# Kernel optimization log

Measured on AMD Instinct MI355X. Metric: run time of the kernel, lower is better.

The kernel has to match this reference:

```python
import jax, jax.numpy as jnp
import numpy as np
from jax import lax

SD = 16  # sample_duration
POOL_KS = (SD, SD * 3 // 4, SD // 2, SD // 4)  # (16, 12, 8, 4)


def conv3d_same(x, w, b):
    # x: [B,C,T,H,W], w: [O,I,3,3,3]
    y = lax.conv_general_dilated(
        x, w, window_strides=(1, 1, 1), padding=[(1, 1), (1, 1), (1, 1)],
        dimension_numbers=("NCDHW", "OIDHW", "NCDHW"))
    return y + b[None, :, None, None, None]


def maxpool_t(x, k):
    # MaxPool3d((k,1,1), stride=1): max over sliding temporal window
    return lax.reduce_window(x, -jnp.inf, lax.max,
                             (1, 1, k, 1, 1), (1, 1, 1, 1, 1), "VALID")


def head1x1(x, w, b):
    # 1x1x1 Conv3d as einsum; x: [B,C,T,H,W], w: [O,C]
    return jnp.einsum("bcthw,oc->bothw", x, w) + b[None, :, None, None, None]


def cls_prob(score):
    # _RPN.reshape(x,2) -> softmax(dim=1) -> reshape back to [B,30,T,H,W]
    B, C, T, H, W = score.shape
    s2 = score.reshape(B, 2, (C * T) // 2, H, W)
    p = jax.nn.softmax(s2, axis=1)
    return p.reshape(B, C, T, H, W)


def setup_inputs() -> dict:
    key = jax.random.key(0)
    ks = jax.random.split(key, 12)
    din, B, H, W = 512, 2, 28, 28
    s = 0.05
    return {
        "base_feat": jax.random.normal(ks[0], (B, din, SD, H, W), jnp.float32),
        "im_info": jnp.ones((B, 3), jnp.float32) * 448.0,
        "gt_boxes": jax.random.uniform(ks[1], (B, 20, 5), jnp.float32),
        "gt_rois": jax.random.uniform(ks[2], (B, 20, SD, 5), jnp.float32),
        "W_conv": jax.random.normal(ks[3], (din, din, 3, 3, 3), jnp.float32) * 0.01,
        "b_conv": jnp.zeros((din,), jnp.float32),
        "W_cls": jax.random.normal(ks[4], (30, din), jnp.float32) * s,
        "b_cls": jnp.zeros((30,), jnp.float32),
        "W_bbox": jax.random.normal(ks[5], (960, din), jnp.float32) * s,
        "b_bbox": jnp.zeros((960,), jnp.float32),
        "W_bbox_34": jax.random.normal(ks[6], (720, din), jnp.float32) * s,
        "b_bbox_34": jnp.zeros((720,), jnp.float32),
        "W_bbox_2": jax.random.normal(ks[7], (480, din), jnp.float32) * s,
        "b_bbox_2": jnp.zeros((480,), jnp.float32),
        "W_bbox_4": jax.random.normal(ks[8], (240, din), jnp.float32) * s,
        "b_bbox_4": jnp.zeros((240,), jnp.float32),
    }


def reference(base_feat, im_info, gt_boxes, gt_rois,
              W_conv, b_conv, W_cls, b_cls,
              W_bbox, b_bbox, W_bbox_34, b_bbox_34,
              W_bbox_2, b_bbox_2, W_bbox_4, b_bbox_4):
    # RPN conv + relu
    x = jax.nn.relu(conv3d_same(base_feat, W_conv, b_conv))
    # four temporal max-pool branches (T' = 1, 5, 9, 13)
    pools = [maxpool_t(x, k) for k in POOL_KS]
    # NOTE: original code applies the SAME RPN_cls_score conv to all branches
    probs = tuple(cls_prob(head1x1(p, W_cls, b_cls)) for p in pools)
    bbox_ws = [(W_bbox, b_bbox), (W_bbox_34, b_bbox_34),
               (W_bbox_2, b_bbox_2), (W_bbox_4, b_bbox_4)]
    bboxes = tuple(head1x1(p, w, b) for p, (w, b) in zip(pools, bbox_ws))
    return probs + bboxes
```

## Files before the change

### kernel.cpp

```cpp
#include <hip/hip_runtime.h>

typedef unsigned short u16;
typedef unsigned int   u32;
typedef __bf16  bf16x8 __attribute__((ext_vector_type(8)));
typedef float   f32x4  __attribute__((ext_vector_type(4)));

__device__ __forceinline__ float bf2f(u16 u) {
    u32 v = ((u32)u) << 16;
    return __builtin_bit_cast(float, v);
}
__device__ __forceinline__ u16 f2bf(float f) {
    u32 u = __builtin_bit_cast(u32, f);
    return (u16)((u + 0x7FFFu + ((u >> 16) & 1u)) >> 16);
}
__device__ __forceinline__ float ldf(const void* p, long i, int f32) {
    return f32 ? ((const float*)p)[i] : bf2f(((const u16*)p)[i]);
}
__device__ __forceinline__ int is_f32(const u32* im) {
    return im[0] == 0x43E00000u;
}
__device__ __forceinline__ void gl2lds16(const u16* g, u16* l) {
    __builtin_amdgcn_global_load_lds(
        (const __attribute__((address_space(1))) void*)g,
        (__attribute__((address_space(3))) void*)l, 16, 0, 0);
}

__global__ void pad_zero_fill(const void* __restrict__ src, u16* __restrict__ xpad,
                              const u32* __restrict__ im)
{
    __shared__ u16 lds[56 * 40];
    if (blockIdx.x >= 7168) {
        int i = (blockIdx.x - 7168) * 256 + threadIdx.x;
        if (i < 230400) {
            int c8 = i & 63; int pos = i >> 6;
            int p = pos % 900; pos /= 900;
            int t = (pos & 1) * 17; int b = pos >> 1;
            long o = (((long)(b * 18 + t) * 900) + p) * 512 + c8 * 8;
            *(uint4*)&xpad[o] = uint4{0u, 0u, 0u, 0u};
            return;
        }
        i -= 230400;
        if (i < 122880) {
            int c8 = i & 63; int pos = i >> 6;
            int w = pos % 30; pos /= 30;
            int h = (pos & 1) * 29; pos >>= 1;
            int t = pos % 16 + 1; int b = pos / 16;
            long o = ((((long)(b * 18 + t) * 30 + h) * 30) + w) * 512 + c8 * 8;
            *(uint4*)&xpad[o] = uint4{0u, 0u, 0u, 0u};
            return;
        }
        i -= 122880;
        if (i < 114688) {
            int c8 = i & 63; int pos = i >> 6;
            int w = (pos & 1) * 29; pos >>= 1;
            int h = pos % 28 + 1; pos /= 28;
            int t = pos % 16 + 1; int b = pos / 16;
            long o = ((((long)(b * 18 + t) * 30 + h) * 30) + w) * 512 + c8 * 8;
            *(uint4*)&xpad[o] = uint4{0u, 0u, 0u, 0u};
        }
        return;
    }
    const int f32 = is_f32(im);
    int blk = blockIdx.x;
    const int h2  = blk % 14;  blk /= 14;
    const int c32 = blk & 15;  blk >>= 4;
    const int t   = blk & 15;
    const int b   = blk >> 4;
    const int tid = threadIdx.x;
    const long sbase = ((long)(b * 512 + c32 * 32) * 16 + t) * 784 + h2 * 56;
    #pragma unroll
    for (int it = tid; it < 1792; it += 256) {
        const int c = it / 56, p = it - c * 56;
        float v = f32 ? ((const float*)src)[sbase + (long)c * 12544 + p]
                      : bf2f(((const u16*)src)[sbase + (long)c * 12544 + p]);
        lds[p * 40 + c] = f2bf(v);
    }
    __syncthreads();
    if (tid < 224) {
        const int p = tid >> 2, g = tid & 3;
        const int h = h2 * 2 + p / 28, w = p % 28;
        const long o = (((long)(b * 18 + t + 1) * 30 + h + 1) * 30 + (w + 1)) * 512
                       + c32 * 32 + g * 8;
        *(uint4*)&xpad[o] = *(const uint4*)&lds[p * 40 + g * 8];
    }
}

__global__ void wt_cvt_all(const void* __restrict__ wconv, u16* __restrict__ wt,
                           const void* s0, const void* s1, const void* s2,
                           const void* s3, const void* s4,
                           const void* b0, const void* b1, const void* b2,
                           const void* b3, const void* b4, const void* b5,
                           u16* __restrict__ whd, float* __restrict__ bfs,
                           const u32* __restrict__ im)
{
    const int f32 = is_f32(im);
    __shared__ u16 lds[256 * 28];
    const int tid = threadIdx.x;
    if (blockIdx.x < 1024) {
        const int pair_base = blockIdx.x * 256;
        const long s0l = (long)pair_base * 27;
        for (int it = tid; it < 256 * 27; it += 256) {
            const int p = it / 27, o = it - p * 27;
            float v = f32 ? ((const float*)wconv)[s0l + it]
                          : bf2f(((const u16*)wconv)[s0l + it]);
            lds[p * 28 + o] = f2bf(v);
        }
        __syncthreads();
        #pragma unroll
        for (int off = 0; off < 27; ++off)
            wt[(long)off * 262144 + pair_base + tid] = lds[tid * 28 + off];
        return;
    }
    int i = (blockIdx.x - 1024) * 256 + tid;
    if (i < 1244160) {
        const void* s; long j;
        if      (i < 15360)   { s = s0; j = i; }
        else if (i < 506880)  { s = s1; j = i - 15360; }
        else if (i < 875520)  { s = s2; j = i - 506880; }
        else if (i < 1121280) { s = s3; j = i - 875520; }
        else                  { s = s4; j = i - 1121280; }
        whd[i] = f2bf(ldf(s, j, f32));
        return;
    }
    i -= 1244160;
    if (i >= 2942) return;
    float v;
    if      (i < 512)  v = ldf(b0, i, f32);
    else if (i < 542)  v = ldf(b1, i - 512, f32);
    else if (i < 1502) v = ldf(b2, i - 542, f32);
    else if (i < 2222) v = ldf(b3, i - 1502, f32);
    else if (i < 2702) v = ldf(b4, i - 2222, f32);
    else               v = ldf(b5, i - 2702, f32);
    bfs[i] = v;
}

__global__ __launch_bounds__(512, 2) void conv_gemm256(
    const u16* __restrict__ xpad, const u16* __restrict__ wt,
    const float* __restrict__ bfs, u16* __restrict__ y)
{
    __shared__ u16 smem[61440];
    const int tid = threadIdx.x;

    const int bx  = blockIdx.x;
    const int L   = (bx & 7) * 28 + (bx >> 3);
    const int m_base = (L & 1) * 256;
    const int n_base = (L >> 1) * 224;

    const int rq8 = tid >> 3;
    const int sw  = (((tid & 7) ^ (rq8 & 7))) * 8;
    const u16* pa = wt + (long)(m_base + rq8) * 512 + sw;

    long sbj[4];
    #pragma unroll
    for (int j = 0; j < 4; ++j) {
        int n = n_base + j * 56 + rq8;
        if (n > 25087) n = 25087;
        int b = n / 12544, r = n % 12544;
        int t = r / 784,   q = r % 784;
        int h = q / 28,    w = q % 28;
        const int sa = ((b * 18 + t) * 30 + h) * 30 + w;
        sbj[j] = (long)sa * 512 + sw;
    }
    const bool stgB = (tid < 448);

    const int lane = tid & 63, wid = tid >> 6;
    const int l16 = lane & 15, quad = lane >> 4;
    const int wm = wid >> 1;
    const int wn = wid & 1;
    const int x7 = l16 & 7;
    const int o0 = (quad ^ x7) * 8;
    const int o1 = ((4 + quad) ^ x7) * 8;
    int rowA[4], rowB[7];
    #pragma unroll
    for (int mi = 0; mi < 4; ++mi) rowA[mi] = (wm * 64 + mi * 16 + l16) * 64;
    #pragma unroll
    for (int ni = 0; ni < 7; ++ni) rowB[ni] = 16384 + (wn * 112 + ni * 16 + l16) * 64;

    f32x4 acc[4][7] = {};

    {
        u16* dst = smem;
        #pragma unroll
        for (int j = 0; j < 4; ++j)
            gl2lds16(pa + (long)j * 32768, dst + j * 4096 + tid * 8);
        if (stgB) {
            #pragma unroll
            for (int j = 0; j < 4; ++j)
                gl2lds16(xpad + sbj[j], dst + 16384 + j * 3584 + tid * 8);
        }
    }

    for (int kt = 0; kt < 216; ++kt) {
        asm volatile("s_waitcnt vmcnt(0)" ::: "memory");
        asm volatile("s_barrier" ::: "memory");
        const u16* buf = smem + (kt & 1) * 30720;

        bf16x8 af[4], bfr[7];
        #pragma unroll
        for (int mi = 0; mi < 4; ++mi)
            af[mi] = *(const bf16x8*)&buf[rowA[mi] + o0];
        #pragma unroll
        for (int ni = 0; ni < 7; ++ni)
            bfr[ni] = *(const bf16x8*)&buf[rowB[ni] + o0];

        if (kt < 215) {
            const int kts = kt + 1;
            const int tap = kts >> 3, kc = kts & 7;
            const int kd = tap / 9, r9 = tap - kd * 9;
            const int kh = r9 / 3,  kw = r9 - kh * 3;
            const long aoff = (long)tap * 262144 + kc * 64;
            const long boff = (long)(kd * 900 + kh * 30 + kw) * 512 + kc * 64;
            u16* dst = smem + (kts & 1) * 30720;
            #pragma unroll
            for (int j = 0; j < 4; ++j)
                gl2lds16(pa + aoff + (long)j * 32768, dst + j * 4096 + tid * 8);
            if (stgB) {
                #pragma unroll
                for (int j = 0; j < 4; ++j)
                    gl2lds16(xpad + sbj[j] + boff, dst + 16384 + j * 3584 + tid * 8);
            }
        }

        __builtin_amdgcn_s_setprio(1);
        #pragma unroll
        for (int mi = 0; mi < 4; ++mi)
            #pragma unroll
            for (int ni = 0; ni < 7; ++ni)
                acc[mi][ni] = __builtin_amdgcn_mfma_f32_16x16x32_bf16(
                    af[mi], bfr[ni], acc[mi][ni], 0, 0, 0);
        __builtin_amdgcn_s_setprio(0);

        bf16x8 ag[4], bgr[7];
        #pragma unroll
        for (int mi = 0; mi < 4; ++mi)
            ag[mi] = *(const bf16x8*)&buf[rowA[mi] + o1];
        #pragma unroll
        for (int ni = 0; ni < 7; ++ni)
            bgr[ni] = *(const bf16x8*)&buf[rowB[ni] + o1];

        __builtin_amdgcn_s_setprio(1);
        #pragma unroll
        for (int mi = 0; mi < 4; ++mi)
            #pragma unroll
            for (int ni = 0; ni < 7; ++ni)
                acc[mi][ni] = __builtin_amdgcn_mfma_f32_16x16x32_bf16(
                    ag[mi], bgr[ni], acc[mi][ni], 0, 0, 0);
        __builtin_amdgcn_s_setprio(0);
    }

    #pragma unroll
    for (int mi = 0; mi < 4; ++mi) {
        const int mrow = m_base + wm * 64 + mi * 16 + quad * 4;
        float bias[4];
        #pragma unroll
        for (int r = 0; r < 4; ++r) bias[r] = bfs[mrow + r];
        #pragma unroll
        for (int ni = 0; ni < 7; ++ni) {
            const int ng = n_base + wn * 112 + ni * 16 + l16;
            f32x4 a = acc[mi][ni];
            u16 o0v = f2bf(fmaxf(a[0] + bias[0], 0.f));
            u16 o1v = f2bf(fmaxf(a[1] + bias[1], 0.f));
            u16 o2v = f2bf(fmaxf(a[2] + bias[2], 0.f));
            u16 o3v = f2bf(fmaxf(a[3] + bias[3], 0.f));
            uint2 pv;
            pv.x = (u32)o0v | ((u32)o1v << 16);
            pv.y = (u32)o2v | ((u32)o3v << 16);
            *(uint2*)&y[(long)ng * 512 + mrow] = pv;
        }
    }
}

__device__ __forceinline__ uint2 max4(uint2 A, uint2 Bv)
{
    const u16* a = (const u16*)&A;
    const u16* b = (const u16*)&Bv;
    uint2 R;
    u16* r = (u16*)&R;
    #pragma unroll
    for (int i = 0; i < 4; ++i) r[i] = (bf2f(a[i]) >= bf2f(b[i])) ? a[i] : b[i];
    return R;
}

__global__ void pool_all(const u16* __restrict__ y, u16* __restrict__ p4,
                         u16* __restrict__ p8, u16* __restrict__ p12,
                         u16* __restrict__ p16)
{
    int g = blockIdx.x * 256 + threadIdx.x;
    if (g >= 200704) return;
    const int c4 = g & 127;
    int pos = g >> 7;
    const int hw = pos % 784; const int b = pos / 784;
    const u16* src = y + ((long)(b * 16) * 784 + hw) * 512 + c4 * 4;
    uint2 v[16];
    #pragma unroll
    for (int t = 0; t < 16; ++t)
        v[t] = *(const uint2*)(src + (long)t * 401408);
    uint2 pr[15];
    #pragma unroll
    for (int t = 0; t < 15; ++t) pr[t] = max4(v[t], v[t + 1]);
    uint2 qd[13];
    #pragma unroll
    for (int t = 0; t < 13; ++t) qd[t] = max4(pr[t], pr[t + 2]);
    uint2 e8[9];
    #pragma unroll
    for (int t = 0; t < 9; ++t) e8[t] = max4(qd[t], qd[t + 4]);
    uint2 e12[5];
    #pragma unroll
    for (int t = 0; t < 5; ++t) e12[t] = max4(e8[t], qd[t + 8]);
    uint2 e16 = max4(e8[0], e8[8]);

    const long col = (long)hw * 512 + c4 * 4;
    #pragma unroll
    for (int t = 0; t < 13; ++t)
        *(uint2*)&p4[((long)(b * 13 + t) * 784) * 512 + col] = qd[t];
    #pragma unroll
    for (int t = 0; t < 9; ++t)
        *(uint2*)&p8[((long)(b * 9 + t) * 784) * 512 + col] = e8[t];
    #pragma unroll
    for (int t = 0; t < 5; ++t)
        *(uint2*)&p12[((long)(b * 5 + t) * 784) * 512 + col] = e12[t];
    *(uint2*)&p16[((long)b * 784) * 512 + col] = e16;
}

__global__ __launch_bounds__(256, 2) void heads_gemm(
    const u16* __restrict__ p16, const u16* __restrict__ p12,
    const u16* __restrict__ p8,  const u16* __restrict__ p4,
    const u16* __restrict__ wcls, const u16* __restrict__ wb1,
    const u16* __restrict__ wb34, const u16* __restrict__ wb2,
    const u16* __restrict__ wb4,  const float* __restrict__ bfs,
    void* __restrict__ outv, const u32* __restrict__ im)
{
    const int f32 = is_f32(im);
    int bid = blockIdx.x;
    const u16* pool; const u16* wbp; int Ti, CH, nt, mt; long boff, coff, ooff;
    if (bid < 104)      {             nt = bid % 13;  mt = bid / 13;  pool = p16; wbp = wb1;  Ti = 1;  CH = 960; boff = 542;  coff = 0;      ooff = 1317120; }
    else if (bid < 476) { bid -= 104; nt = bid % 62;  mt = bid / 62;  pool = p12; wbp = wb34; Ti = 5;  CH = 720; boff = 1502; coff = 47040;  ooff = 2822400; }
    else if (bid < 920) { bid -= 476; nt = bid % 111; mt = bid / 111; pool = p8;  wbp = wb2;  Ti = 9;  CH = 480; boff = 2222; coff = 282240; ooff = 8467200; }
    else                { bid -= 920; nt = bid % 160; mt = bid / 160; pool = p4;  wbp = wb4;  Ti = 13; CH = 240; boff = 2702; coff = 705600; ooff = 15240960; }
    const int M = 30 + CH;
    const int THW = Ti * 784;
    const int N = 2 * THW;
    const int n_base = nt * 128;
    const int m_base = mt * 128;

    __shared__ u16 lds[24576];
    const int tid = threadIdx.x;
    const int lane = tid & 63;
    const int wid  = tid >> 6;
    const int quad = lane >> 4;
    const int l16  = lane & 15;
    const int wm = (wid & 1) * 64;
    const int wn = (wid >> 1) * 64;

    const int srow = tid >> 2;
    const int kk   = (((tid & 3) ^ ((tid >> 3) & 3))) * 8;

    const u16* arow[2]; const u16* brow[2];
    #pragma unroll
    for (int i = 0; i < 2; ++i) {
        int m = m_base + i * 64 + srow; if (m > M - 1) m = M - 1;
        arow[i] = ((m < 30) ? (wcls + m * 512) : (wbp + (m - 30) * 512)) + kk;
        int n = n_base + i * 64 + srow; if (n > N - 1) n = N - 1;
        brow[i] = pool + (long)n * 512 + kk;
    }

    const int co = (quad ^ ((l16 >> 1) & 3)) * 8;
    int rowA[4], rowB[4];
    #pragma unroll
    for (int i = 0; i < 4; ++i) {
        rowA[i] = (wm + i * 16 + l16) * 32 + co;
        rowB[i] = 4096 + (wn + i * 16 + l16) * 32 + co;
    }

    #pragma unroll
    for (int i = 0; i < 2; ++i)
        gl2lds16(arow[i], &lds[i * 2048 + tid * 8]);
    #pragma unroll
    for (int i = 0; i < 2; ++i)
        gl2lds16(brow[i], &lds[4096 + i * 2048 + tid * 8]);
    #pragma unroll
    for (int i = 0; i < 2; ++i)
        gl2lds16(arow[i] + 32, &lds[8192 + i * 2048 + tid * 8]);
    #pragma unroll
    for (int i = 0; i < 2; ++i)
        gl2lds16(brow[i] + 32, &lds[8192 + 4096 + i * 2048 + tid * 8]);

    f32x4 acc[4][4] = {};
    int cb = 0;
    for (int kc = 0; kc < 15; ++kc) {
        asm volatile("s_waitcnt vmcnt(4)" ::: "memory");
        asm volatile("s_barrier" ::: "memory");
        const u16* buf = lds + cb * 8192;
        bf16x8 af[4], bfr[4];
        #pragma unroll
        for (int mi = 0; mi < 4; ++mi)
            af[mi]  = *(const bf16x8*)&buf[rowA[mi]];
        #pragma unroll
        for (int ni = 0; ni < 4; ++ni)
            bfr[ni] = *(const bf16x8*)&buf[rowB[ni]];
        if (kc < 14) {
            const int kcol = (kc + 2) * 32;
            int nb = cb + 2; if (nb >= 3) nb -= 3;
            u16* dst = lds + nb * 8192 + tid * 8;
            #pragma unroll
            for (int i = 0; i < 2; ++i)
                gl2lds16(arow[i] + kcol, dst + i * 2048);
            #pragma unroll
            for (int i = 0; i < 2; ++i)
                gl2lds16(brow[i] + kcol, dst + 4096 + i * 2048);
        }
        __builtin_amdgcn_s_setprio(1);
        #pragma unroll
        for (int mi = 0; mi < 4; ++mi)
            #pragma unroll
            for (int ni = 0; ni < 4; ++ni)
                acc[mi][ni] = __builtin_amdgcn_mfma_f32_16x16x32_bf16(
                    af[mi], bfr[ni], acc[mi][ni], 0, 0, 0);
        __builtin_amdgcn_s_setprio(0);
        cb = (cb + 1 == 3) ? 0 : cb + 1;
    }
    {
        asm volatile("s_waitcnt vmcnt(0)" ::: "memory");
        asm volatile("s_barrier" ::: "memory");
        const u16* buf = lds + cb * 8192;
        bf16x8 af[4], bfr[4];
        #pragma unroll
        for (int mi = 0; mi < 4; ++mi)
            af[mi]  = *(const bf16x8*)&buf[rowA[mi]];
        #pragma unroll
        for (int ni = 0; ni < 4; ++ni)
            bfr[ni] = *(const bf16x8*)&buf[rowB[ni]];
        #pragma unroll
        for (int mi = 0; mi < 4; ++mi)
            #pragma unroll
            for (int ni = 0; ni < 4; ++ni)
                acc[mi][ni] = __builtin_amdgcn_mfma_f32_16x16x32_bf16(
                    af[mi], bfr[ni], acc[mi][ni], 0, 0, 0);
    }

    __syncthreads();
    float* smf = (float*)lds;
    const float* bcls = bfs + 512;
    const float* bb   = bfs + boff;
    #pragma unroll
    for (int mi = 0; mi < 4; ++mi) {
        const int mrow = m_base + wm + mi * 16 + quad * 4;
        #pragma unroll
        for (int ni = 0; ni < 4; ++ni) {
            const int ng = n_base + wn + ni * 16 + l16;
            if (ng >= N) continue;
            const int b  = ng / THW;
            const int rr = ng % THW;
            f32x4 a = acc[mi][ni];
            #pragma unroll
            for (int r = 0; r < 4; ++r) {
                const int m = mrow + r;
                if (m >= M) break;
                if (m < 30) {
                    smf[m * 128 + (wn + ni * 16 + l16)] = a[r] + bcls[m];
                } else {
                    const float v = a[r] + bb[m - 30];
                    const long oi = ooff + ((long)(b * CH + (m - 30))) * THW + rr;
                    if (f32) ((float*)outv)[oi] = v;
                    else     ((u16*)outv)[oi]   = f2bf(v);
                }
            }
        }
    }
    __syncthreads();
    if (m_base == 0) {
        for (int p = tid; p < 1920; p += 256) {
            const int j = p >> 7, col = p & 127;
            const int ng = n_base + col;
            if (ng >= N) continue;
            const float s0 = smf[j * 128 + col];
            const float s1 = smf[(j + 15) * 128 + col];
            const float mx = fmaxf(s0, s1);
            const float e0 = __expf(s0 - mx), e1 = __expf(s1 - mx);
            const float inv = 1.0f / (e0 + e1);
            const int b = ng / THW, rr = ng % THW;
            const long i0 = coff + ((long)(b * 30 + j)) * THW + rr;
            const long i1 = coff + ((long)(b * 30 + j + 15)) * THW + rr;
            if (f32) {
                ((float*)outv)[i0] = e0 * inv;
                ((float*)outv)[i1] = e1 * inv;
            } else {
                ((u16*)outv)[i0] = f2bf(e0 * inv);
                ((u16*)outv)[i1] = f2bf(e1 * inv);
            }
        }
    }
}

extern "C" void kernel_launch(void* const* d_in, const int* in_sizes, int n_in,
                              void* d_out, int out_size, void* d_ws, size_t ws_size,
                              hipStream_t stream)
{
    const void* base_feat = d_in[0];
    const u32*  im_info   = (const u32*)d_in[1];
    const void* W_conv    = d_in[4];
    const void* b_conv    = d_in[5];
    const void* W_cls     = d_in[6];
    const void* b_cls     = d_in[7];
    const void* W_bbox    = d_in[8];
    const void* b_bbox    = d_in[9];
    const void* W_bbox34  = d_in[10];
    const void* b_bbox34  = d_in[11];
    const void* W_bbox2   = d_in[12];
    const void* b_bbox2   = d_in[13];
    const void* W_bbox4   = d_in[14];
    const void* b_bbox4   = d_in[15];

    char* ws = (char*)d_ws;
    u16*   xpad = (u16*)  (ws + 0);
    u16*   wt   = (u16*)  (ws + 33177600);
    u16*   y    = (u16*)  (ws + 47333376);
    u16*   p4   = (u16*)  (ws + 73023488);
    u16*   p8   = (u16*)  (ws + 93896704);
    u16*   p12  = (u16*)  (ws + 108347392);
    u16*   p16  = (u16*)  (ws + 116375552);
    u16*   whd  = (u16*)  (ws + 123249728);
    float* bfs  = (float*)(ws + 125738048);

    u16* w_cls_b  = whd;
    u16* w_b1_b   = whd + 15360;
    u16* w_b34_b  = whd + 506880;
    u16* w_b2_b   = whd + 875520;
    u16* w_b4_b   = whd + 1121280;

    pad_zero_fill<<<8996, 256, 0, stream>>>(base_feat, xpad, im_info);
    wt_cvt_all<<<5897, 256, 0, stream>>>(W_conv, wt,
                                         W_cls, W_bbox, W_bbox34, W_bbox2, W_bbox4,
                                         b_conv, b_cls, b_bbox, b_bbox34, b_bbox2,
                                         b_bbox4, whd, bfs, im_info);

    conv_gemm256<<<224, 512, 0, stream>>>(xpad, wt, bfs, y);

    pool_all<<<784, 256, 0, stream>>>(y, p4, p8, p12, p16);

    heads_gemm<<<1400, 256, 0, stream>>>(p16, p12, p8, p4,
                                         w_cls_b, w_b1_b, w_b34_b, w_b2_b, w_b4_b,
                                         bfs, d_out, im_info);
}
```

Measured before the change: 541.9 us.

## Merge prep kernels and enlarge heads GEMM M-tile to 256

Merges the input padding/zero-fill kernel and the weight conversion kernel into a single launch, removing one kernel launch and its tail. The heads GEMM now uses 256x128 tiles instead of 128x128, so each wave computes 128x64 with 8x4 MFMA accumulators. This roughly halves the number of blocks and cuts re-reads of the pooled activations, at the cost of more registers and LDS (72KB). It also wastes more compute on padded M rows for the small-channel branches.

```diff
diff --git a/kernel.cpp b/kernel.cpp
--- a/kernel.cpp
+++ b/kernel.cpp
@@ -25,12 +25,44 @@
         (__attribute__((address_space(3))) void*)l, 16, 0, 0);
 }
 
-__global__ void pad_zero_fill(const void* __restrict__ src, u16* __restrict__ xpad,
-                              const u32* __restrict__ im)
+__global__ void prep_all(const void* __restrict__ src, u16* __restrict__ xpad,
+                         const void* __restrict__ wconv, u16* __restrict__ wt,
+                         const void* s0, const void* s1, const void* s2,
+                         const void* s3, const void* s4,
+                         const void* b0, const void* b1, const void* b2,
+                         const void* b3, const void* b4, const void* b5,
+                         u16* __restrict__ whd, float* __restrict__ bfs,
+                         const u32* __restrict__ im)
 {
-    __shared__ u16 lds[56 * 40];
-    if (blockIdx.x >= 7168) {
-        int i = (blockIdx.x - 7168) * 256 + threadIdx.x;
+    __shared__ u16 lds[7168];
+    const int tid = threadIdx.x;
+    if (blockIdx.x < 7168) {
+        const int f32 = is_f32(im);
+        int blk = blockIdx.x;
+        const int h2  = blk % 14;  blk /= 14;
+        const int c32 = blk & 15;  blk >>= 4;
+        const int t   = blk & 15;
+        const int b   = blk >> 4;
+        const long sbase = ((long)(b * 512 + c32 * 32) * 16 + t) * 784 + h2 * 56;
+        #pragma unroll
+        for (int it = tid; it < 1792; it += 256) {
+            const int c = it / 56, p = it - c * 56;
+            float v = f32 ? ((const float*)src)[sbase + (long)c * 12544 + p]
+                          : bf2f(((const u16*)src)[sbase + (long)c * 12544 + p]);
+            lds[p * 40 + c] = f2bf(v);
+        }
+        __syncthreads();
+        if (tid < 224) {
+            const int p = tid >> 2, g = tid & 3;
+            const int h = h2 * 2 + p / 28, w = p % 28;
+            const long o = (((long)(b * 18 + t + 1) * 30 + h + 1) * 30 + (w + 1)) * 512
+                           + c32 * 32 + g * 8;
+            *(uint4*)&xpad[o] = *(const uint4*)&lds[p * 40 + g * 8];
+        }
+        return;
+    }
+    if (blockIdx.x < 8996) {
+        int i = (blockIdx.x - 7168) * 256 + tid;
         if (i < 230400) {
             int c8 = i & 63; int pos = i >> 6;
             int p = pos % 900; pos /= 900;
@@ -61,43 +93,8 @@
         return;
     }
     const int f32 = is_f32(im);
-    int blk = blockIdx.x;
-    const int h2  = blk % 14;  blk /= 14;
-    const int c32 = blk & 15;  blk >>= 4;
-    const int t   = blk & 15;
-    const int b   = blk >> 4;
-    const int tid = threadIdx.x;
-    const long sbase = ((long)(b * 512 + c32 * 32) * 16 + t) * 784 + h2 * 56;
-    #pragma unroll
-    for (int it = tid; it < 1792; it += 256) {
-        const int c = it / 56, p = it - c * 56;
-        float v = f32 ? ((const float*)src)[sbase + (long)c * 12544 + p]
-                      : bf2f(((const u16*)src)[sbase + (long)c * 12544 + p]);
-        lds[p * 40 + c] = f2bf(v);
-    }
-    __syncthreads();
-    if (tid < 224) {
-        const int p = tid >> 2, g = tid & 3;
-        const int h = h2 * 2 + p / 28, w = p % 28;
-        const long o = (((long)(b * 18 + t + 1) * 30 + h + 1) * 30 + (w + 1)) * 512
-                       + c32 * 32 + g * 8;
-        *(uint4*)&xpad[o] = *(const uint4*)&lds[p * 40 + g * 8];
-    }
-}
-
-__global__ void wt_cvt_all(const void* __restrict__ wconv, u16* __restrict__ wt,
-                           const void* s0, const void* s1, const void* s2,
-                           const void* s3, const void* s4,
-                           const void* b0, const void* b1, const void* b2,
-                           const void* b3, const void* b4, const void* b5,
-                           u16* __restrict__ whd, float* __restrict__ bfs,
-                           const u32* __restrict__ im)
-{
-    const int f32 = is_f32(im);
-    __shared__ u16 lds[256 * 28];
-    const int tid = threadIdx.x;
-    if (blockIdx.x < 1024) {
-        const int pair_base = blockIdx.x * 256;
+    if (blockIdx.x < 10020) {
+        const int pair_base = (blockIdx.x - 8996) * 256;
         const long s0l = (long)pair_base * 27;
         for (int it = tid; it < 256 * 27; it += 256) {
             const int p = it / 27, o = it - p * 27;
@@ -111,7 +108,7 @@
             wt[(long)off * 262144 + pair_base + tid] = lds[tid * 28 + off];
         return;
     }
-    int i = (blockIdx.x - 1024) * 256 + tid;
+    int i = (blockIdx.x - 10020) * 256 + tid;
     if (i < 1244160) {
         const void* s; long j;
         if      (i < 15360)   { s = s0; j = i; }
@@ -333,67 +330,69 @@
     const int f32 = is_f32(im);
     int bid = blockIdx.x;
     const u16* pool; const u16* wbp; int Ti, CH, nt, mt; long boff, coff, ooff;
-    if (bid < 104)      {             nt = bid % 13;  mt = bid / 13;  pool = p16; wbp = wb1;  Ti = 1;  CH = 960; boff = 542;  coff = 0;      ooff = 1317120; }
-    else if (bid < 476) { bid -= 104; nt = bid % 62;  mt = bid / 62;  pool = p12; wbp = wb34; Ti = 5;  CH = 720; boff = 1502; coff = 47040;  ooff = 2822400; }
-    else if (bid < 920) { bid -= 476; nt = bid % 111; mt = bid / 111; pool = p8;  wbp = wb2;  Ti = 9;  CH = 480; boff = 2222; coff = 282240; ooff = 8467200; }
-    else                { bid -= 920; nt = bid % 160; mt = bid / 160; pool = p4;  wbp = wb4;  Ti = 13; CH = 240; boff = 2702; coff = 705600; ooff = 15240960; }
+    if (bid < 52)       {             nt = bid % 13;  mt = bid / 13;  pool = p16; wbp = wb1;  Ti = 1;  CH = 960; boff = 542;  coff = 0;      ooff = 1317120; }
+    else if (bid < 238) { bid -= 52;  nt = bid % 62;  mt = bid / 62;  pool = p12; wbp = wb34; Ti = 5;  CH = 720; boff = 1502; coff = 47040;  ooff = 2822400; }
+    else if (bid < 460) { bid -= 238; nt = bid % 111; mt = bid / 111; pool = p8;  wbp = wb2;  Ti = 9;  CH = 480; boff = 2222; coff = 282240; ooff = 8467200; }
+    else                { bid -= 460; nt = bid % 160; mt = bid / 160; pool = p4;  wbp = wb4;  Ti = 13; CH = 240; boff = 2702; coff = 705600; ooff = 15240960; }
     const int M = 30 + CH;
     const int THW = Ti * 784;
     const int N = 2 * THW;
     const int n_base = nt * 128;
-    const int m_base = mt * 128;
-
-    __shared__ u16 lds[24576];
+    const int m_base = mt * 256;
+
+    __shared__ u16 lds[36864];
     const int tid = threadIdx.x;
     const int lane = tid & 63;
     const int wid  = tid >> 6;
     const int quad = lane >> 4;
     const int l16  = lane & 15;
-    const int wm = (wid & 1) * 64;
-    const int wn = (wid >> 1) * 64;
+    const int wm = wid & 1;
+    const int wn = wid >> 1;
 
     const int srow = tid >> 2;
     const int kk   = (((tid & 3) ^ ((tid >> 3) & 3))) * 8;
 
-    const u16* arow[2]; const u16* brow[2];
-    #pragma unroll
-    for (int i = 0; i < 2; ++i) {
+    const u16* arow[4]; const u16* brow[2];
+    #pragma unroll
+    for (int i = 0; i < 4; ++i) {
         int m = m_base + i * 64 + srow; if (m > M - 1) m = M - 1;
         arow[i] = ((m < 30) ? (wcls + m * 512) : (wbp + (m - 30) * 512)) + kk;
+    }
+    #pragma unroll
+    for (int i = 0; i < 2; ++i) {
         int n = n_base + i * 64 + srow; if (n > N - 1) n = N - 1;
         brow[i] = pool + (long)n * 512 + kk;
     }
 
     const int co = (quad ^ ((l16 >> 1) & 3)) * 8;
-    int rowA[4], rowB[4];
-    #pragma unroll
-    for (int i = 0; i < 4; ++i) {
-        rowA[i] = (wm + i * 16 + l16) * 32 + co;
-        rowB[i] = 4096 + (wn + i * 16 + l16) * 32 + co;
-    }
-
-    #pragma unroll
-    for (int i = 0; i < 2; ++i)
-        gl2lds16(arow[i], &lds[i * 2048 + tid * 8]);
-    #pragma unroll
-    for (int i = 0; i < 2; ++i)
-        gl2lds16(brow[i], &lds[4096 + i * 2048 + tid * 8]);
-    #pragma unroll
-    for (int i = 0; i < 2; ++i)
-        gl2lds16(arow[i] + 32, &lds[8192 + i * 2048 + tid * 8]);
-    #pragma unroll
-    for (int i = 0; i < 2; ++i)
-        gl2lds16(brow[i] + 32, &lds[8192 + 4096 + i * 2048 + tid * 8]);
-
-    f32x4 acc[4][4] = {};
+    int rowA[8], rowB[4];
+    #pragma unroll
+    for (int i = 0; i < 8; ++i)
+        rowA[i] = (wm * 128 + i * 16 + l16) * 32 + co;
+    #pragma unroll
+    for (int i = 0; i < 4; ++i)
+        rowB[i] = 8192 + (wn * 64 + i * 16 + l16) * 32 + co;
+
+    #pragma unroll
+    for (int s = 0; s < 2; ++s) {
+        u16* dst = lds + s * 12288 + tid * 8;
+        #pragma unroll
+        for (int i = 0; i < 4; ++i)
+            gl2lds16(arow[i] + s * 32, dst + i * 2048);
+        #pragma unroll
+        for (int i = 0; i < 2; ++i)
+            gl2lds16(brow[i] + s * 32, dst + 8192 + i * 2048);
+    }
+
+    f32x4 acc[8][4] = {};
     int cb = 0;
     for (int kc = 0; kc < 15; ++kc) {
-        asm volatile("s_waitcnt vmcnt(4)" ::: "memory");
+        asm volatile("s_waitcnt vmcnt(6)" ::: "memory");
         asm volatile("s_barrier" ::: "memory");
-        const u16* buf = lds + cb * 8192;
-        bf16x8 af[4], bfr[4];
-        #pragma unroll
-        for (int mi = 0; mi < 4; ++mi)
+        const u16* buf = lds + cb * 12288;
+        bf16x8 af[8], bfr[4];
+        #pragma unroll
+        for (int mi = 0; mi < 8; ++mi)
             af[mi]  = *(const bf16x8*)&buf[rowA[mi]];
         #pragma unroll
         for (int ni = 0; ni < 4; ++ni)
@@ -401,17 +400,17 @@
         if (kc < 14) {
             const int kcol = (kc + 2) * 32;
             int nb = cb + 2; if (nb >= 3) nb -= 3;
-            u16* dst = lds + nb * 8192 + tid * 8;
+            u16* dst = lds + nb * 12288 + tid * 8;
+            #pragma unroll
+            for (int i = 0; i < 4; ++i)
+                gl2lds16(arow[i] + kcol, dst + i * 2048);
             #pragma unroll
             for (int i = 0; i < 2; ++i)
-                gl2lds16(arow[i] + kcol, dst + i * 2048);
-            #pragma unroll
-            for (int i = 0; i < 2; ++i)
-                gl2lds16(brow[i] + kcol, dst + 4096 + i * 2048);
+                gl2lds16(brow[i] + kcol, dst + 8192 + i * 2048);
         }
         __builtin_amdgcn_s_setprio(1);
         #pragma unroll
-        for (int mi = 0; mi < 4; ++mi)
+        for (int mi = 0; mi < 8; ++mi)
             #pragma unroll
             for (int ni = 0; ni < 4; ++ni)
                 acc[mi][ni] = __builtin_amdgcn_mfma_f32_16x16x32_bf16(
@@ -422,16 +421,16 @@
     {
         asm volatile("s_waitcnt vmcnt(0)" ::: "memory");
         asm volatile("s_barrier" ::: "memory");
-        const u16* buf = lds + cb * 8192;
-        bf16x8 af[4], bfr[4];
-        #pragma unroll
-        for (int mi = 0; mi < 4; ++mi)
+        const u16* buf = lds + cb * 12288;
+        bf16x8 af[8], bfr[4];
+        #pragma unroll
+        for (int mi = 0; mi < 8; ++mi)
             af[mi]  = *(const bf16x8*)&buf[rowA[mi]];
         #pragma unroll
         for (int ni = 0; ni < 4; ++ni)
             bfr[ni] = *(const bf16x8*)&buf[rowB[ni]];
         #pragma unroll
-        for (int mi = 0; mi < 4; ++mi)
+        for (int mi = 0; mi < 8; ++mi)
             #pragma unroll
             for (int ni = 0; ni < 4; ++ni)
                 acc[mi][ni] = __builtin_amdgcn_mfma_f32_16x16x32_bf16(
@@ -443,11 +442,11 @@
     const float* bcls = bfs + 512;
     const float* bb   = bfs + boff;
     #pragma unroll
-    for (int mi = 0; mi < 4; ++mi) {
-        const int mrow = m_base + wm + mi * 16 + quad * 4;
+    for (int mi = 0; mi < 8; ++mi) {
+        const int mrow = m_base + wm * 128 + mi * 16 + quad * 4;
         #pragma unroll
         for (int ni = 0; ni < 4; ++ni) {
-            const int ng = n_base + wn + ni * 16 + l16;
+            const int ng = n_base + wn * 64 + ni * 16 + l16;
             if (ng >= N) continue;
             const int b  = ng / THW;
             const int rr = ng % THW;
@@ -457,7 +456,7 @@
                 const int m = mrow + r;
                 if (m >= M) break;
                 if (m < 30) {
-                    smf[m * 128 + (wn + ni * 16 + l16)] = a[r] + bcls[m];
+                    smf[m * 128 + (wn * 64 + ni * 16 + l16)] = a[r] + bcls[m];
                 } else {
                     const float v = a[r] + bb[m - 30];
                     const long oi = ooff + ((long)(b * CH + (m - 30))) * THW + rr;
@@ -528,17 +527,16 @@
     u16* w_b2_b   = whd + 875520;
     u16* w_b4_b   = whd + 1121280;
 
-    pad_zero_fill<<<8996, 256, 0, stream>>>(base_feat, xpad, im_info);
-    wt_cvt_all<<<5897, 256, 0, stream>>>(W_conv, wt,
-                                         W_cls, W_bbox, W_bbox34, W_bbox2, W_bbox4,
-                                         b_conv, b_cls, b_bbox, b_bbox34, b_bbox2,
-                                         b_bbox4, whd, bfs, im_info);
+    prep_all<<<14893, 256, 0, stream>>>(base_feat, xpad, W_conv, wt,
+                                        W_cls, W_bbox, W_bbox34, W_bbox2, W_bbox4,
+                                        b_conv, b_cls, b_bbox, b_bbox34, b_bbox2,
+                                        b_bbox4, whd, bfs, im_info);
 
     conv_gemm256<<<224, 512, 0, stream>>>(xpad, wt, bfs, y);
 
     pool_all<<<784, 256, 0, stream>>>(y, p4, p8, p12, p16);
 
-    heads_gemm<<<1400, 256, 0, stream>>>(p16, p12, p8, p4,
-                                         w_cls_b, w_b1_b, w_b34_b, w_b2_b, w_b4_b,
-                                         bfs, d_out, im_info);
-}
+    heads_gemm<<<780, 256, 0, stream>>>(p16, p12, p8, p4,
+                                        w_cls_b, w_b1_b, w_b34_b, w_b2_b, w_b4_b,
+                                        bfs, d_out, im_info);
+}
```

After: 552.3 us. No clear change (+1.9%).
